# Performance work log

Hardware: AMD Instinct MI355X
Metric: run time of the kernel (lower is better)

Reference implementation:

```python
import jax, jax.numpy as jnp
import numpy as np

N_NODES = 50000
N_EDGES = 800000
D_IN = 128
D_OUT = 128


def setup_inputs() -> dict:
    key = jax.random.key(0)
    k = jax.random.split(key, 6)
    x = jax.random.normal(k[0], (N_NODES, D_IN), dtype=jnp.float32)
    weight = jax.random.normal(k[1], (D_IN, D_OUT), dtype=jnp.float32) * (1.0 / np.sqrt(D_IN))
    bias = jax.random.normal(k[2], (D_OUT,), dtype=jnp.float32)
    src = jax.random.randint(k[3], (N_EDGES,), 0, N_NODES, dtype=jnp.int32)
    dst = jax.random.randint(k[4], (N_EDGES,), 0, N_NODES, dtype=jnp.int32)
    edge_vals = jax.random.uniform(k[5], (N_EDGES,), dtype=jnp.float32)
    return {"x": x, "weight": weight, "bias": bias, "src": src, "dst": dst, "edge_vals": edge_vals}


def reference(x, weight, bias, src, dst, edge_vals):
    # support = x @ W  (dense projection), [N, D_OUT]
    support = jnp.matmul(x, weight)
    # spmm: out[d] = sum_{e: dst[e]==d} edge_vals[e] * support[src[e]]
    msgs = support[src] * edge_vals[:, None]  # [E, D_OUT]
    out = jax.ops.segment_sum(msgs, dst, num_segments=x.shape[0])
    return out + bias
```

## Files before the change

kernel.cpp:

```cpp
#include <hip/hip_runtime.h>
#include <hip/hip_bf16.h>

#define D 128
#define BKT 32
#define CAP 768
#define SC_EPB 4096
#define NBMAX 1600

typedef __attribute__((ext_vector_type(8))) short bf16x8;
typedef __attribute__((ext_vector_type(4))) float f32x4;

__device__ __forceinline__ unsigned short f2bf(float f) {
  union { float f; unsigned u; } c; c.f = f;
  unsigned u = c.u + 0x7FFFu + ((c.u >> 16) & 1u);
  return (unsigned short)(u >> 16);
}
__device__ __forceinline__ float bf_lo(unsigned u) {
  union { unsigned u; float f; } c; c.u = u << 16; return c.f;
}
__device__ __forceinline__ float bf_hi(unsigned u) {
  union { unsigned u; float f; } c; c.u = u & 0xFFFF0000u; return c.f;
}

#define EV_Q 2047.0f
#define EV_IQ (1.0f / 2047.0f)

__global__ __launch_bounds__(256) void setup(
    const float* __restrict__ w, unsigned short* __restrict__ wT,
    int* __restrict__ bcur, int nb) {
  const int idx = blockIdx.x * 256 + threadIdx.x;
  if (idx < D * D) {
    const int k = idx >> 7, n = idx & 127;
    wT[n * D + k] = f2bf(w[idx]);
  }
  if (idx < nb) bcur[idx] = 0;
}

__global__ __launch_bounds__(512) void fused_scatter_gemm(
    const float* __restrict__ x, const unsigned short* __restrict__ wT,
    unsigned short* __restrict__ supb, int n_nodes,
    const int* __restrict__ src, const int* __restrict__ dst,
    const float* __restrict__ ev, int* __restrict__ bcur,
    unsigned* __restrict__ staged, int n_edges, int nb, int gemm_blocks) {
  __shared__ char smem[2 * 64 * 136 * 2];
  const int t = threadIdx.x;

  if ((int)blockIdx.x < gemm_blocks) {
    const int sub = t >> 8;
    const int t256 = t & 255;
    unsigned short* xs = (unsigned short*)smem + sub * (64 * 136);
    const int row0 = blockIdx.x * 128 + sub * 64;

    for (int f = t256; f < 64 * 32; f += 256) {
      const int r = f >> 5, c4 = f & 31;
      const int gr = row0 + r;
      float4 v = make_float4(0.f, 0.f, 0.f, 0.f);
      if (gr < n_nodes) v = ((const float4*)(x + (size_t)gr * D))[c4];
      ushort4 b;
      b.x = f2bf(v.x); b.y = f2bf(v.y); b.z = f2bf(v.z); b.w = f2bf(v.w);
      *(ushort4*)(&xs[r * 136 + c4 * 4]) = b;
    }
    __syncthreads();

    const int wv = t256 >> 6;
    const int lane = t256 & 63;
    const int l15 = lane & 15;
    const int quad = lane >> 4;

    f32x4 acc[8];
#pragma unroll
    for (int q = 0; q < 8; q++) acc[q] = (f32x4){0.f, 0.f, 0.f, 0.f};

#pragma unroll
    for (int k0 = 0; k0 < D; k0 += 32) {
      const bf16x8 a =
          *(const bf16x8*)(&xs[(wv * 16 + l15) * 136 + k0 + quad * 8]);
      const unsigned short* wp = wT + (size_t)l15 * D + k0 + quad * 8;
#pragma unroll
      for (int q = 0; q < 8; q++) {
        const bf16x8 b = *(const bf16x8*)(wp + (size_t)q * 16 * D);
        acc[q] = __builtin_amdgcn_mfma_f32_16x16x32_bf16(a, b, acc[q], 0, 0, 0);
      }
    }

#pragma unroll
    for (int q = 0; q < 8; q++) {
      const int col = q * 16 + l15;
#pragma unroll
      for (int r = 0; r < 4; r++) {
        const int row = row0 + wv * 16 + quad * 4 + r;
        if (row < n_nodes) supb[(size_t)row * D + col] = f2bf(acc[q][r]);
      }
    }
  } else {
    int* hist = (int*)smem;
    int* cur = hist + NBMAX;
    const int base = ((int)blockIdx.x - gemm_blocks) * SC_EPB;
    const int cnt = min(SC_EPB, n_edges - base);

    for (int i = t; i < nb; i += 512) hist[i] = 0;
    __syncthreads();
    for (int j = t; j < cnt; j += 512) atomicAdd(&hist[dst[base + j] >> 5], 1);
    __syncthreads();
    for (int i = t; i < nb; i += 512) {
      const int h = hist[i];
      cur[i] = h ? atomicAdd(&bcur[i], h) : 0;
    }
    __syncthreads();
    for (int j = t; j < cnt; j += 512) {
      const int e = base + j;
      const int d = dst[e];
      const int b = d >> 5;
      const int p = atomicAdd(&cur[b], 1);
      if (p < CAP) {
        const unsigned evq = (unsigned)__float2int_rn(ev[e] * EV_Q);
        staged[(size_t)b * CAP + p] =
            ((unsigned)src[e] << 16) | ((unsigned)(d & 31) << 11) | evq;
      }
    }
  }
}

__global__ __launch_bounds__(512) void bucket_reduce(
    const unsigned short* __restrict__ supb, const unsigned* __restrict__ staged,
    const int* __restrict__ bcnt, const float* __restrict__ bias,
    float* __restrict__ out, int n_nodes) {
  __shared__ unsigned rec[CAP];
  __shared__ unsigned ordered[CAP];
  __shared__ int hist[BKT];
  __shared__ int segbase[BKT];
  __shared__ int cur[BKT];

  const int t = threadIdx.x;
  const int b = blockIdx.x;
  const int lo = b << 5;
  const int cnt = min(bcnt[b], CAP);
  const unsigned* st = staged + (size_t)b * CAP;

  if (t < BKT) hist[t] = 0;
  __syncthreads();
  for (int j = t; j < cnt; j += 512) {
    const unsigned p = st[j];
    rec[j] = p;
    atomicAdd(&hist[(p >> 11) & 31], 1);
  }
  __syncthreads();
  if (t < BKT) {
    const int h = hist[t];
    int incl = h;
#pragma unroll
    for (int ofs = 1; ofs < BKT; ofs <<= 1) {
      const int v = __shfl_up(incl, ofs, 64);
      if (t >= ofs) incl += v;
    }
    segbase[t] = incl - h;
    cur[t] = incl - h;
  }
  __syncthreads();
  for (int j = t; j < cnt; j += 512) {
    const unsigned p = rec[j];
    const int pos = atomicAdd(&cur[(p >> 11) & 31], 1);
    ordered[pos] = p;
  }
  __syncthreads();

  const int n = t >> 4;
  const int p = t & 15;
  const int beg = segbase[n];
  const int end = beg + hist[n];

  float a[8];
#pragma unroll
  for (int k = 0; k < 8; k++) a[k] = 0.f;

  int j = beg;
  for (; j + 4 <= end; j += 4) {
    const unsigned pr0 = ordered[j];
    const unsigned pr1 = ordered[j + 1];
    const unsigned pr2 = ordered[j + 2];
    const unsigned pr3 = ordered[j + 3];
    const uint4 r0 = ((const uint4*)(supb + (size_t)(pr0 >> 16) * D))[p];
    const uint4 r1 = ((const uint4*)(supb + (size_t)(pr1 >> 16) * D))[p];
    const uint4 r2 = ((const uint4*)(supb + (size_t)(pr2 >> 16) * D))[p];
    const uint4 r3 = ((const uint4*)(supb + (size_t)(pr3 >> 16) * D))[p];
    const float v0 = (float)(pr0 & 2047u) * EV_IQ;
    const float v1 = (float)(pr1 & 2047u) * EV_IQ;
    const float v2 = (float)(pr2 & 2047u) * EV_IQ;
    const float v3 = (float)(pr3 & 2047u) * EV_IQ;
    a[0] += v0 * bf_lo(r0.x) + v1 * bf_lo(r1.x) + v2 * bf_lo(r2.x) + v3 * bf_lo(r3.x);
    a[1] += v0 * bf_hi(r0.x) + v1 * bf_hi(r1.x) + v2 * bf_hi(r2.x) + v3 * bf_hi(r3.x);
    a[2] += v0 * bf_lo(r0.y) + v1 * bf_lo(r1.y) + v2 * bf_lo(r2.y) + v3 * bf_lo(r3.y);
    a[3] += v0 * bf_hi(r0.y) + v1 * bf_hi(r1.y) + v2 * bf_hi(r2.y) + v3 * bf_hi(r3.y);
    a[4] += v0 * bf_lo(r0.z) + v1 * bf_lo(r1.z) + v2 * bf_lo(r2.z) + v3 * bf_lo(r3.z);
    a[5] += v0 * bf_hi(r0.z) + v1 * bf_hi(r1.z) + v2 * bf_hi(r2.z) + v3 * bf_hi(r3.z);
    a[6] += v0 * bf_lo(r0.w) + v1 * bf_lo(r1.w) + v2 * bf_lo(r2.w) + v3 * bf_lo(r3.w);
    a[7] += v0 * bf_hi(r0.w) + v1 * bf_hi(r1.w) + v2 * bf_hi(r2.w) + v3 * bf_hi(r3.w);
  }
  for (; j < end; j++) {
    const unsigned pr0 = ordered[j];
    const uint4 r0 = ((const uint4*)(supb + (size_t)(pr0 >> 16) * D))[p];
    const float v0 = (float)(pr0 & 2047u) * EV_IQ;
    a[0] += v0 * bf_lo(r0.x);
    a[1] += v0 * bf_hi(r0.x);
    a[2] += v0 * bf_lo(r0.y);
    a[3] += v0 * bf_hi(r0.y);
    a[4] += v0 * bf_lo(r0.z);
    a[5] += v0 * bf_hi(r0.z);
    a[6] += v0 * bf_lo(r0.w);
    a[7] += v0 * bf_hi(r0.w);
  }

  const int node = lo + n;
  if (node < n_nodes) {
    const float4 bv0 = ((const float4*)bias)[p * 2];
    const float4 bv1 = ((const float4*)bias)[p * 2 + 1];
    float4* op = (float4*)out + (size_t)node * 32 + p * 2;
    op[0] = make_float4(a[0] + bv0.x, a[1] + bv0.y, a[2] + bv0.z, a[3] + bv0.w);
    op[1] = make_float4(a[4] + bv1.x, a[5] + bv1.y, a[6] + bv1.z, a[7] + bv1.w);
  }
}

extern "C" void kernel_launch(void* const* d_in, const int* in_sizes, int n_in,
                              void* d_out, int out_size, void* d_ws, size_t ws_size,
                              hipStream_t stream) {
  const float* x    = (const float*)d_in[0];
  const float* w    = (const float*)d_in[1];
  const float* bias = (const float*)d_in[2];
  const int*   src  = (const int*)d_in[3];
  const int*   dst  = (const int*)d_in[4];
  const float* ev   = (const float*)d_in[5];
  float* out = (float*)d_out;

  const int n_nodes = in_sizes[0] / D;
  const int n_edges = in_sizes[3];
  const int nb = (n_nodes + BKT - 1) / BKT;

  unsigned short* supb = (unsigned short*)d_ws;
  unsigned short* wT = supb + (size_t)n_nodes * D;
  int* bcur = (int*)(wT + D * D);
  unsigned* staged = (unsigned*)(bcur + NBMAX);

  setup<<<64, 256, 0, stream>>>(w, wT, bcur, nb);

  const int gemm_blocks = (n_nodes + 127) / 128;
  const int scat_blocks = (n_edges + SC_EPB - 1) / SC_EPB;
  fused_scatter_gemm<<<gemm_blocks + scat_blocks, 512, 0, stream>>>(
      x, wT, supb, n_nodes, src, dst, ev, bcur, staged, n_edges, nb,
      gemm_blocks);

  bucket_reduce<<<nb, 512, 0, stream>>>(supb, staged, bcur, bias, out, n_nodes);
}
```

Measured before the change: 146.2 us.

## Balance bucket_reduce work by splitting edges evenly with shared-memory atomic flushes

In bucket_reduce, each 16-thread group used to handle all edges of one destination node, so work per group varied with node degree. Now the sorted edge list of a bucket is split into 32 equal slices, and partial sums are flushed into a shared-memory accumulator with atomics whenever the destination node changes. This evens out load across the block at the cost of LDS atomics, an extra 16KB of shared memory and a further barrier. The scatter stage also doubles its edges per block, giving fewer blocks with more work each.

```diff
diff --git a/kernel.cpp b/kernel.cpp
--- a/kernel.cpp
+++ b/kernel.cpp
@@ -4,7 +4,7 @@
 #define D 128
 #define BKT 32
 #define CAP 768
-#define SC_EPB 4096
+#define SC_EPB 8192
 #define NBMAX 1600
 
 typedef __attribute__((ext_vector_type(8))) short bf16x8;
@@ -128,8 +128,8 @@
   __shared__ unsigned rec[CAP];
   __shared__ unsigned ordered[CAP];
   __shared__ int hist[BKT];
-  __shared__ int segbase[BKT];
   __shared__ int cur[BKT];
+  __shared__ float accs[BKT][D];
 
   const int t = threadIdx.x;
   const int b = blockIdx.x;
@@ -138,6 +138,12 @@
   const unsigned* st = staged + (size_t)b * CAP;
 
   if (t < BKT) hist[t] = 0;
+  {
+    float4* az = (float4*)&accs[0][0];
+    const float4 z4 = make_float4(0.f, 0.f, 0.f, 0.f);
+    az[t] = z4;
+    az[t + 512] = z4;
+  }
   __syncthreads();
   for (int j = t; j < cnt; j += 512) {
     const unsigned p = st[j];
@@ -153,7 +159,6 @@
       const int v = __shfl_up(incl, ofs, 64);
       if (t >= ofs) incl += v;
     }
-    segbase[t] = incl - h;
     cur[t] = incl - h;
   }
   __syncthreads();
@@ -164,17 +169,44 @@
   }
   __syncthreads();
 
-  const int n = t >> 4;
   const int p = t & 15;
-  const int beg = segbase[n];
-  const int end = beg + hist[n];
+  const int s = t >> 4;
+  int j = (cnt * s) >> 5;
+  const int jend = (cnt * (s + 1)) >> 5;
 
   float a[8];
 #pragma unroll
   for (int k = 0; k < 8; k++) a[k] = 0.f;
-
-  int j = beg;
-  for (; j + 4 <= end; j += 4) {
+  int curnode = -1;
+
+#define FLUSH()                                                         \
+  {                                                                     \
+    _Pragma("unroll") for (int k = 0; k < 8; k++) {                     \
+      const int kk = (k + p) & 7;                                       \
+      atomicAdd(&accs[curnode][p * 8 + kk], a[kk]);                     \
+      a[kk] = 0.f;                                                      \
+    }                                                                   \
+  }
+
+#define PROC(pr, r)                                                     \
+  {                                                                     \
+    const int nd_ = (int)(((pr) >> 11) & 31);                           \
+    if (nd_ != curnode) {                                               \
+      if (curnode >= 0) FLUSH();                                        \
+      curnode = nd_;                                                    \
+    }                                                                   \
+    const float v_ = (float)((pr) & 2047u) * EV_IQ;                     \
+    a[0] += v_ * bf_lo((r).x);                                          \
+    a[1] += v_ * bf_hi((r).x);                                          \
+    a[2] += v_ * bf_lo((r).y);                                          \
+    a[3] += v_ * bf_hi((r).y);                                          \
+    a[4] += v_ * bf_lo((r).z);                                          \
+    a[5] += v_ * bf_hi((r).z);                                          \
+    a[6] += v_ * bf_lo((r).w);                                          \
+    a[7] += v_ * bf_hi((r).w);                                          \
+  }
+
+  for (; j + 4 <= jend; j += 4) {
     const unsigned pr0 = ordered[j];
     const unsigned pr1 = ordered[j + 1];
     const unsigned pr2 = ordered[j + 2];
@@ -183,40 +215,31 @@
     const uint4 r1 = ((const uint4*)(supb + (size_t)(pr1 >> 16) * D))[p];
     const uint4 r2 = ((const uint4*)(supb + (size_t)(pr2 >> 16) * D))[p];
     const uint4 r3 = ((const uint4*)(supb + (size_t)(pr3 >> 16) * D))[p];
-    const float v0 = (float)(pr0 & 2047u) * EV_IQ;
-    const float v1 = (float)(pr1 & 2047u) * EV_IQ;
-    const float v2 = (float)(pr2 & 2047u) * EV_IQ;
-    const float v3 = (float)(pr3 & 2047u) * EV_IQ;
-    a[0] += v0 * bf_lo(r0.x) + v1 * bf_lo(r1.x) + v2 * bf_lo(r2.x) + v3 * bf_lo(r3.x);
-    a[1] += v0 * bf_hi(r0.x) + v1 * bf_hi(r1.x) + v2 * bf_hi(r2.x) + v3 * bf_hi(r3.x);
-    a[2] += v0 * bf_lo(r0.y) + v1 * bf_lo(r1.y) + v2 * bf_lo(r2.y) + v3 * bf_lo(r3.y);
-    a[3] += v0 * bf_hi(r0.y) + v1 * bf_hi(r1.y) + v2 * bf_hi(r2.y) + v3 * bf_hi(r3.y);
-    a[4] += v0 * bf_lo(r0.z) + v1 * bf_lo(r1.z) + v2 * bf_lo(r2.z) + v3 * bf_lo(r3.z);
-    a[5] += v0 * bf_hi(r0.z) + v1 * bf_hi(r1.z) + v2 * bf_hi(r2.z) + v3 * bf_hi(r3.z);
-    a[6] += v0 * bf_lo(r0.w) + v1 * bf_lo(r1.w) + v2 * bf_lo(r2.w) + v3 * bf_lo(r3.w);
-    a[7] += v0 * bf_hi(r0.w) + v1 * bf_hi(r1.w) + v2 * bf_hi(r2.w) + v3 * bf_hi(r3.w);
-  }
-  for (; j < end; j++) {
+    PROC(pr0, r0);
+    PROC(pr1, r1);
+    PROC(pr2, r2);
+    PROC(pr3, r3);
+  }
+  for (; j < jend; j++) {
     const unsigned pr0 = ordered[j];
     const uint4 r0 = ((const uint4*)(supb + (size_t)(pr0 >> 16) * D))[p];
-    const float v0 = (float)(pr0 & 2047u) * EV_IQ;
-    a[0] += v0 * bf_lo(r0.x);
-    a[1] += v0 * bf_hi(r0.x);
-    a[2] += v0 * bf_lo(r0.y);
-    a[3] += v0 * bf_hi(r0.y);
-    a[4] += v0 * bf_lo(r0.z);
-    a[5] += v0 * bf_hi(r0.z);
-    a[6] += v0 * bf_lo(r0.w);
-    a[7] += v0 * bf_hi(r0.w);
-  }
-
+    PROC(pr0, r0);
+  }
+  if (curnode >= 0) FLUSH();
+#undef PROC
+#undef FLUSH
+  __syncthreads();
+
+  const int n = t >> 4;
   const int node = lo + n;
   if (node < n_nodes) {
     const float4 bv0 = ((const float4*)bias)[p * 2];
     const float4 bv1 = ((const float4*)bias)[p * 2 + 1];
+    const float4 s0 = *(const float4*)&accs[n][p * 8];
+    const float4 s1 = *(const float4*)&accs[n][p * 8 + 4];
     float4* op = (float4*)out + (size_t)node * 32 + p * 2;
-    op[0] = make_float4(a[0] + bv0.x, a[1] + bv0.y, a[2] + bv0.z, a[3] + bv0.w);
-    op[1] = make_float4(a[4] + bv1.x, a[5] + bv1.y, a[6] + bv1.z, a[7] + bv1.w);
+    op[0] = make_float4(s0.x + bv0.x, s0.y + bv0.y, s0.z + bv0.z, s0.w + bv0.w);
+    op[1] = make_float4(s1.x + bv1.x, s1.y + bv1.y, s1.z + bv1.z, s1.w + bv1.w);
   }
 }
 
```

Measured after the change: 197.5 us. 1.35x slower.

## Split each node's edge list across two 8-lane groups in bucket reduce

Applied to the files above, without the earlier changes.

The gather-reduce in bucket_reduce now assigns each node two groups of 8 threads. Each thread loads 32 bytes (two uint4) per edge row and handles alternating edges, and the two partial sums are combined through a padded shared-memory buffer before the bias is added and the output written. The goal is more bytes per load and two independent edge streams per node, to improve memory-level parallelism for the random row gathers. In exchange it doubles accumulator registers, adds an LDS exchange and a barrier, and writes are now done by half the threads. The scatter edges-per-block is also doubled, which halves the number of scatter blocks and their global bucket-cursor atomics.

```diff
diff --git a/kernel.cpp b/kernel.cpp
--- a/kernel.cpp
+++ b/kernel.cpp
@@ -4,8 +4,9 @@
 #define D 128
 #define BKT 32
 #define CAP 768
-#define SC_EPB 4096
+#define SC_EPB 8192
 #define NBMAX 1600
+#define CPAD 4
 
 typedef __attribute__((ext_vector_type(8))) short bf16x8;
 typedef __attribute__((ext_vector_type(4))) float f32x4;
@@ -130,6 +131,7 @@
   __shared__ int hist[BKT];
   __shared__ int segbase[BKT];
   __shared__ int cur[BKT];
+  __shared__ float comb[BKT][D + CPAD];
 
   const int t = threadIdx.x;
   const int b = blockIdx.x;
@@ -165,58 +167,70 @@
   __syncthreads();
 
   const int n = t >> 4;
-  const int p = t & 15;
+  const int h = (t >> 3) & 1;
+  const int p8 = t & 7;
   const int beg = segbase[n];
   const int end = beg + hist[n];
 
-  float a[8];
-#pragma unroll
-  for (int k = 0; k < 8; k++) a[k] = 0.f;
-
-  int j = beg;
-  for (; j + 4 <= end; j += 4) {
+  float a[16];
+#pragma unroll
+  for (int k = 0; k < 16; k++) a[k] = 0.f;
+
+#define PROC1(pr, ra, rb)                                               \
+  {                                                                     \
+    const float v_ = (float)((pr) & 2047u) * EV_IQ;                     \
+    a[0] += v_ * bf_lo((ra).x);  a[1] += v_ * bf_hi((ra).x);            \
+    a[2] += v_ * bf_lo((ra).y);  a[3] += v_ * bf_hi((ra).y);            \
+    a[4] += v_ * bf_lo((ra).z);  a[5] += v_ * bf_hi((ra).z);            \
+    a[6] += v_ * bf_lo((ra).w);  a[7] += v_ * bf_hi((ra).w);            \
+    a[8] += v_ * bf_lo((rb).x);  a[9] += v_ * bf_hi((rb).x);            \
+    a[10] += v_ * bf_lo((rb).y); a[11] += v_ * bf_hi((rb).y);           \
+    a[12] += v_ * bf_lo((rb).z); a[13] += v_ * bf_hi((rb).z);           \
+    a[14] += v_ * bf_lo((rb).w); a[15] += v_ * bf_hi((rb).w);           \
+  }
+
+  int j = beg + h;
+  for (; j + 2 < end; j += 4) {
     const unsigned pr0 = ordered[j];
-    const unsigned pr1 = ordered[j + 1];
-    const unsigned pr2 = ordered[j + 2];
-    const unsigned pr3 = ordered[j + 3];
-    const uint4 r0 = ((const uint4*)(supb + (size_t)(pr0 >> 16) * D))[p];
-    const uint4 r1 = ((const uint4*)(supb + (size_t)(pr1 >> 16) * D))[p];
-    const uint4 r2 = ((const uint4*)(supb + (size_t)(pr2 >> 16) * D))[p];
-    const uint4 r3 = ((const uint4*)(supb + (size_t)(pr3 >> 16) * D))[p];
-    const float v0 = (float)(pr0 & 2047u) * EV_IQ;
-    const float v1 = (float)(pr1 & 2047u) * EV_IQ;
-    const float v2 = (float)(pr2 & 2047u) * EV_IQ;
-    const float v3 = (float)(pr3 & 2047u) * EV_IQ;
-    a[0] += v0 * bf_lo(r0.x) + v1 * bf_lo(r1.x) + v2 * bf_lo(r2.x) + v3 * bf_lo(r3.x);
-    a[1] += v0 * bf_hi(r0.x) + v1 * bf_hi(r1.x) + v2 * bf_hi(r2.x) + v3 * bf_hi(r3.x);
-    a[2] += v0 * bf_lo(r0.y) + v1 * bf_lo(r1.y) + v2 * bf_lo(r2.y) + v3 * bf_lo(r3.y);
-    a[3] += v0 * bf_hi(r0.y) + v1 * bf_hi(r1.y) + v2 * bf_hi(r2.y) + v3 * bf_hi(r3.y);
-    a[4] += v0 * bf_lo(r0.z) + v1 * bf_lo(r1.z) + v2 * bf_lo(r2.z) + v3 * bf_lo(r3.z);
-    a[5] += v0 * bf_hi(r0.z) + v1 * bf_hi(r1.z) + v2 * bf_hi(r2.z) + v3 * bf_hi(r3.z);
-    a[6] += v0 * bf_lo(r0.w) + v1 * bf_lo(r1.w) + v2 * bf_lo(r2.w) + v3 * bf_lo(r3.w);
-    a[7] += v0 * bf_hi(r0.w) + v1 * bf_hi(r1.w) + v2 * bf_hi(r2.w) + v3 * bf_hi(r3.w);
-  }
-  for (; j < end; j++) {
+    const unsigned pr1 = ordered[j + 2];
+    const uint4* rp0 = (const uint4*)(supb + (size_t)(pr0 >> 16) * D);
+    const uint4* rp1 = (const uint4*)(supb + (size_t)(pr1 >> 16) * D);
+    const uint4 r0a = rp0[p8 * 2];
+    const uint4 r0b = rp0[p8 * 2 + 1];
+    const uint4 r1a = rp1[p8 * 2];
+    const uint4 r1b = rp1[p8 * 2 + 1];
+    PROC1(pr0, r0a, r0b);
+    PROC1(pr1, r1a, r1b);
+  }
+  for (; j < end; j += 2) {
     const unsigned pr0 = ordered[j];
-    const uint4 r0 = ((const uint4*)(supb + (size_t)(pr0 >> 16) * D))[p];
-    const float v0 = (float)(pr0 & 2047u) * EV_IQ;
-    a[0] += v0 * bf_lo(r0.x);
-    a[1] += v0 * bf_hi(r0.x);
-    a[2] += v0 * bf_lo(r0.y);
-    a[3] += v0 * bf_hi(r0.y);
-    a[4] += v0 * bf_lo(r0.z);
-    a[5] += v0 * bf_hi(r0.z);
-    a[6] += v0 * bf_lo(r0.w);
-    a[7] += v0 * bf_hi(r0.w);
-  }
+    const uint4* rp0 = (const uint4*)(supb + (size_t)(pr0 >> 16) * D);
+    const uint4 r0a = rp0[p8 * 2];
+    const uint4 r0b = rp0[p8 * 2 + 1];
+    PROC1(pr0, r0a, r0b);
+  }
+#undef PROC1
+
+  if (h == 1) {
+#pragma unroll
+    for (int q = 0; q < 4; q++)
+      *(float4*)&comb[n][p8 * 16 + q * 4] =
+          make_float4(a[q * 4], a[q * 4 + 1], a[q * 4 + 2], a[q * 4 + 3]);
+  }
+  __syncthreads();
 
   const int node = lo + n;
-  if (node < n_nodes) {
-    const float4 bv0 = ((const float4*)bias)[p * 2];
-    const float4 bv1 = ((const float4*)bias)[p * 2 + 1];
-    float4* op = (float4*)out + (size_t)node * 32 + p * 2;
-    op[0] = make_float4(a[0] + bv0.x, a[1] + bv0.y, a[2] + bv0.z, a[3] + bv0.w);
-    op[1] = make_float4(a[4] + bv1.x, a[5] + bv1.y, a[6] + bv1.z, a[7] + bv1.w);
+  if (h == 0 && node < n_nodes) {
+#pragma unroll
+    for (int q = 0; q < 4; q++) {
+      const float4 cv = *(const float4*)&comb[n][p8 * 16 + q * 4];
+      const float4 bv = ((const float4*)bias)[p8 * 4 + q];
+      float4* op = (float4*)out + (size_t)node * 32 + p8 * 4 + q;
+      *op = make_float4(a[q * 4] + cv.x + bv.x,
+                        a[q * 4 + 1] + cv.y + bv.y,
+                        a[q * 4 + 2] + cv.z + bv.z,
+                        a[q * 4 + 3] + cv.w + bv.w);
+    }
   }
 }
 
```

New measurement: 146.8 us. About the same (+0.4%).
